# Kernel tuning notes

Hardware: AMD Instinct MI355X
Metric: run time of the kernel (lower is better)

## Reference

```python
import jax, jax.numpy as jnp
import numpy as np

B = 8        # graphs per batch
VG = 20000   # vertices per graph
K = 128      # eigenvectors per graph
D = 128      # channels (C_inout)
V = B * VG


def setup_inputs() -> dict:
    key = jax.random.key(0)
    kx, km, ke, kv, kt = jax.random.split(key, 5)
    x = jax.random.normal(kx, (V, D), dtype=jnp.float32)
    # lumped (diagonal) mass, positive
    mass = jax.random.uniform(km, (V,), dtype=jnp.float32, minval=0.5, maxval=1.5)
    # per-graph nonnegative eigenvalues, sorted within each graph, stacked to (B*K,)
    evals = jnp.sort(jax.random.uniform(ke, (B, K), dtype=jnp.float32) * 10.0, axis=1).reshape(-1)
    # eigenbasis, roughly mass-orthonormal scale
    evecs = jax.random.normal(kv, (V, K), dtype=jnp.float32) / np.sqrt(VG)
    # learned per-channel diffusion times, positive
    diffusion_time = jax.random.uniform(kt, (D,), dtype=jnp.float32, minval=0.01, maxval=0.2)
    batch = jnp.repeat(jnp.arange(B, dtype=jnp.int32), VG)
    return {"x": x, "mass": mass, "evals": evals, "evecs": evecs,
            "diffusion_time": diffusion_time, "batch": batch, "bs": B}


def reference(x, mass, evals, evecs, diffusion_time, batch, bs):
    Vtot, Dc = x.shape
    neig = evals.shape[0] // bs
    vg = Vtot // bs  # equal-sized graphs -> ragged grouped matmul == batched matmul
    t = jnp.maximum(diffusion_time, 1e-8)  # torch clamp(min=1e-8)
    xb = x.reshape(bs, vg, Dc)            # (B, Vg, D)
    eb = evecs.reshape(bs, vg, neig)      # (B, Vg, K)
    mb = mass.reshape(bs, vg)             # (B, Vg) diagonal mass
    # to_basis: basis^T @ (M x) per graph -> (B, K, D)
    x_spec = jnp.einsum('bvk,bvd->bkd', eb * mb[..., None], xb)
    # spectral diffusion coefficients exp(-lambda * t_c): (B, K, D)
    coefs = jnp.exp(-evals.reshape(bs, neig)[..., None] * t[None, None, :])
    # from_basis: evecs @ (coefs * x_spec) per graph -> (B, Vg, D)
    x_diffuse = jnp.einsum('bvk,bkd->bvd', eb, coefs * x_spec)
    return x_diffuse.reshape(Vtot, Dc)
```

## Files before the change

### kernel.cpp

```cpp
#include <hip/hip_runtime.h>

#define BGR 8
#define VG  20000
#define NK  128
#define ND  128

typedef float f32x4 __attribute__((ext_vector_type(4)));
typedef short bf16x8 __attribute__((ext_vector_type(8)));

__device__ __forceinline__ short bf16r(float f) {
    union { float f; unsigned u; } c; c.f = f;
    unsigned r = (c.u + 0x7FFFu + ((c.u >> 16) & 1u)) >> 16;
    return (short)r;
}

#define VC 320
#define S1 40

__global__ __launch_bounds__(256) void k_spec(const float* __restrict__ x,
                                              const float* __restrict__ mass,
                                              const float* __restrict__ evecs,
                                              float* __restrict__ xs) {
    const int g     = blockIdx.y;
    const int chunk = blockIdx.x;
    const int v0    = chunk * VC;
    const int rounds = (VG - v0 < VC ? VG - v0 : VC) >> 5;

    const float* xg = x     + (size_t)g * VG * ND;
    const float* eg = evecs + (size_t)g * VG * NK;
    const float* mg = mass  + (size_t)g * VG;

    __shared__ short At[NK * S1];
    __shared__ short Bt[ND * S1];

    const int tid = threadIdx.x;
    const int l   = tid & 63;
    const int w   = tid >> 6;
    const int lo  = l & 15, hi = l >> 4;
    const int r0  = (w & 1) * 64, c0 = (w >> 1) * 64;

    f32x4 acc[4][4] = {};

    for (int r = 0; r < rounds; ++r) {
        const int vb = v0 + r * 32;
#pragma unroll
        for (int it = 0; it < 8; ++it) {
            const int v = it * 4 + w;
            const float  m  = mg[vb + v];
            const float2 xv = *(const float2*)(xg + (size_t)(vb + v) * ND + 2 * l);
            const float2 ev = *(const float2*)(eg + (size_t)(vb + v) * NK + 2 * l);
            Bt[(2 * l + 0) * S1 + v] = bf16r(xv.x * m);
            Bt[(2 * l + 1) * S1 + v] = bf16r(xv.y * m);
            At[(2 * l + 0) * S1 + v] = bf16r(ev.x);
            At[(2 * l + 1) * S1 + v] = bf16r(ev.y);
        }
        __syncthreads();

        bf16x8 af[4], bfv[4];
#pragma unroll
        for (int i = 0; i < 4; ++i)
            af[i] = *(const bf16x8*)(At + (r0 + 16 * i + lo) * S1 + hi * 8);
#pragma unroll
        for (int j = 0; j < 4; ++j)
            bfv[j] = *(const bf16x8*)(Bt + (c0 + 16 * j + lo) * S1 + hi * 8);
#pragma unroll
        for (int i = 0; i < 4; ++i)
#pragma unroll
            for (int j = 0; j < 4; ++j)
                acc[i][j] = __builtin_amdgcn_mfma_f32_16x16x32_bf16(af[i], bfv[j], acc[i][j], 0, 0, 0);
        __syncthreads();
    }

    float* og = xs + (size_t)g * NK * ND;
#pragma unroll
    for (int i = 0; i < 4; ++i)
#pragma unroll
        for (int j = 0; j < 4; ++j)
#pragma unroll
            for (int t = 0; t < 4; ++t) {
                const int kk = r0 + 16 * i + hi * 4 + t;
                const int dd = c0 + 16 * j + lo;
                atomicAdd(og + kk * ND + dd, acc[i][j][t]);
            }
}

__global__ __launch_bounds__(256) void k_coef(const float* __restrict__ xs,
                                              const float* __restrict__ evals,
                                              const float* __restrict__ dt,
                                              short* __restrict__ Yt) {
    const int gid = blockIdx.x * 256 + threadIdx.x;
    const int g = gid >> 14;
    const int d = (gid >> 7) & 127;
    const int k = gid & 127;
    const float t   = fmaxf(dt[d], 1e-8f);
    const float lam = evals[g * NK + k];
    const float v   = xs[(size_t)g * NK * ND + k * ND + d];
    Yt[gid] = bf16r(__expf(-lam * t) * v);
}

#define S2 128

__global__ __launch_bounds__(256) void k_out(const float* __restrict__ evecs,
                                             const short* __restrict__ Yt,
                                             float* __restrict__ out) {
    const int g     = blockIdx.y;
    const int chunk = blockIdx.x;
    const int v0    = chunk * 128;
    const int rows  = (VG - v0 < 128) ? (VG - v0) : 128;

    const float* eg = evecs + (size_t)g * VG * NK;
    float*       og = out   + (size_t)g * VG * ND;
    const short* yg = Yt    + (size_t)g * ND * NK;

    __shared__ short As[128 * S2];
    __shared__ short Bs[128 * S2];

    const int tid = threadIdx.x;
#pragma unroll
    for (int it = 0; it < 16; ++it) {
        const int id = it * 256 + tid;
        const int v  = id >> 5;
        const int c4 = id & 31;
        const int vc = v < rows ? v : rows - 1;
        const float4 e4 = *(const float4*)(eg + (size_t)(v0 + vc) * NK + 4 * c4);
        short4 p;
        p.x = bf16r(e4.x); p.y = bf16r(e4.y); p.z = bf16r(e4.z); p.w = bf16r(e4.w);
        *(short4*)(As + v * S2 + 4 * c4) = p;
        *(uint2*)(Bs + v * S2 + 4 * c4) = *(const uint2*)(yg + v * NK + 4 * c4);
    }
    __syncthreads();

    const int l  = tid & 63;
    const int w  = tid >> 6;
    const int lo = l & 15, hi = l >> 4;
    const int r0 = (w & 1) * 64, c0 = (w >> 1) * 64;

    f32x4 acc[4][4] = {};
#pragma unroll
    for (int ks = 0; ks < 4; ++ks) {
        const int k0 = ks * 32;
        bf16x8 af[4], bfv[4];
#pragma unroll
        for (int i = 0; i < 4; ++i)
            af[i] = *(const bf16x8*)(As + (r0 + 16 * i + lo) * S2 + k0 + hi * 8);
#pragma unroll
        for (int j = 0; j < 4; ++j)
            bfv[j] = *(const bf16x8*)(Bs + (c0 + 16 * j + lo) * S2 + k0 + hi * 8);
#pragma unroll
        for (int i = 0; i < 4; ++i)
#pragma unroll
            for (int j = 0; j < 4; ++j)
                acc[i][j] = __builtin_amdgcn_mfma_f32_16x16x32_bf16(af[i], bfv[j], acc[i][j], 0, 0, 0);
    }

#pragma unroll
    for (int i = 0; i < 4; ++i)
#pragma unroll
        for (int j = 0; j < 4; ++j)
#pragma unroll
            for (int t = 0; t < 4; ++t) {
                const int vv = r0 + 16 * i + hi * 4 + t;
                if (vv < rows)
                    og[(size_t)(v0 + vv) * ND + c0 + 16 * j + lo] = acc[i][j][t];
            }
}

extern "C" void kernel_launch(void* const* d_in, const int* in_sizes, int n_in,
                              void* d_out, int out_size, void* d_ws, size_t ws_size,
                              hipStream_t stream) {
    const float* x     = (const float*)d_in[0];
    const float* mass  = (const float*)d_in[1];
    const float* evals = (const float*)d_in[2];
    const float* evecs = (const float*)d_in[3];
    const float* dt    = (const float*)d_in[4];
    float* out = (float*)d_out;

    float* xs = (float*)d_ws;
    short* Yt = (short*)((char*)d_ws + (size_t)BGR * NK * ND * 4);

    hipMemsetAsync(d_ws, 0, (size_t)BGR * NK * ND * sizeof(float), stream);

    k_spec<<<dim3((VG + VC - 1) / VC, BGR), 256, 0, stream>>>(x, mass, evecs, xs);
    k_coef<<<(BGR * NK * ND) / 256, 256, 0, stream>>>(xs, evals, dt, Yt);
    k_out<<<dim3((VG + 127) / 128, BGR), 256, 0, stream>>>(evecs, Yt, out);
}
```

Measured before the change: 262.1 us.

## Vectorize spectral staging loads, halve chunk size, read Yt fragments directly from global

In the projection kernel, each thread now loads float4 rows for two adjacent vertices and writes packed bf16 pairs into shared memory, replacing scalar float2 loads and 16-bit stores. The vertex chunk drops from 320 to 160 so twice as many blocks run, at the cost of twice as many atomic flushes of the per-chunk partial results. In the output kernel the Yt operand is no longer staged in shared memory; MFMA fragments are read straight from global/L2, and the evecs tile gets a padded stride to reduce LDS bank conflicts. This removes a shared buffer and a barrier-bound copy but makes each wave issue repeated global reads of the small Yt matrix.

Result: slower. 279.6 us (+6.7%).

```diff
diff --git a/kernel.cpp b/kernel.cpp
--- a/kernel.cpp
+++ b/kernel.cpp
@@ -8,23 +8,23 @@
 typedef float f32x4 __attribute__((ext_vector_type(4)));
 typedef short bf16x8 __attribute__((ext_vector_type(8)));
 
-__device__ __forceinline__ short bf16r(float f) {
+__device__ __forceinline__ unsigned short bf16r(float f) {
     union { float f; unsigned u; } c; c.f = f;
-    unsigned r = (c.u + 0x7FFFu + ((c.u >> 16) & 1u)) >> 16;
-    return (short)r;
+    return (unsigned short)((c.u + 0x7FFFu + ((c.u >> 16) & 1u)) >> 16);
+}
+__device__ __forceinline__ unsigned pack2(float a, float b) {
+    return (unsigned)bf16r(a) | ((unsigned)bf16r(b) << 16);
 }
 
-#define VC 320
+#define VC 160
 #define S1 40
 
 __global__ __launch_bounds__(256) void k_spec(const float* __restrict__ x,
                                               const float* __restrict__ mass,
                                               const float* __restrict__ evecs,
                                               float* __restrict__ xs) {
-    const int g     = blockIdx.y;
-    const int chunk = blockIdx.x;
-    const int v0    = chunk * VC;
-    const int rounds = (VG - v0 < VC ? VG - v0 : VC) >> 5;
+    const int g  = blockIdx.y;
+    const int v0 = blockIdx.x * VC;
 
     const float* xg = x     + (size_t)g * VG * ND;
     const float* eg = evecs + (size_t)g * VG * NK;
@@ -41,18 +41,26 @@
 
     f32x4 acc[4][4] = {};
 
-    for (int r = 0; r < rounds; ++r) {
+#pragma unroll 1
+    for (int r = 0; r < VC / 32; ++r) {
         const int vb = v0 + r * 32;
 #pragma unroll
-        for (int it = 0; it < 8; ++it) {
-            const int v = it * 4 + w;
-            const float  m  = mg[vb + v];
-            const float2 xv = *(const float2*)(xg + (size_t)(vb + v) * ND + 2 * l);
-            const float2 ev = *(const float2*)(eg + (size_t)(vb + v) * NK + 2 * l);
-            Bt[(2 * l + 0) * S1 + v] = bf16r(xv.x * m);
-            Bt[(2 * l + 1) * S1 + v] = bf16r(xv.y * m);
-            At[(2 * l + 0) * S1 + v] = bf16r(ev.x);
-            At[(2 * l + 1) * S1 + v] = bf16r(ev.y);
+        for (int it = 0; it < 2; ++it) {
+            const int id = it * 256 + tid;
+            const int vp = id & 15;
+            const int cq = id >> 4;
+            const int v  = vb + 2 * vp;
+            const float2 mm = *(const float2*)(mg + v);
+            const f32x4 xa = *(const f32x4*)(xg + (size_t)v * ND + 4 * cq);
+            const f32x4 xb = *(const f32x4*)(xg + (size_t)(v + 1) * ND + 4 * cq);
+            const f32x4 ea = *(const f32x4*)(eg + (size_t)v * NK + 4 * cq);
+            const f32x4 eb = *(const f32x4*)(eg + (size_t)(v + 1) * NK + 4 * cq);
+#pragma unroll
+            for (int i = 0; i < 4; ++i) {
+                const int c = 4 * cq + i;
+                *(unsigned*)(Bt + c * S1 + 2 * vp) = pack2(xa[i] * mm.x, xb[i] * mm.y);
+                *(unsigned*)(At + c * S1 + 2 * vp) = pack2(ea[i], eb[i]);
+            }
         }
         __syncthreads();
 
@@ -87,7 +95,7 @@
 __global__ __launch_bounds__(256) void k_coef(const float* __restrict__ xs,
                                               const float* __restrict__ evals,
                                               const float* __restrict__ dt,
-                                              short* __restrict__ Yt) {
+                                              unsigned short* __restrict__ Yt) {
     const int gid = blockIdx.x * 256 + threadIdx.x;
     const int g = gid >> 14;
     const int d = (gid >> 7) & 127;
@@ -98,7 +106,7 @@
     Yt[gid] = bf16r(__expf(-lam * t) * v);
 }
 
-#define S2 128
+#define S2 136
 
 __global__ __launch_bounds__(256) void k_out(const float* __restrict__ evecs,
                                              const short* __restrict__ Yt,
@@ -113,7 +121,6 @@
     const short* yg = Yt    + (size_t)g * ND * NK;
 
     __shared__ short As[128 * S2];
-    __shared__ short Bs[128 * S2];
 
     const int tid = threadIdx.x;
 #pragma unroll
@@ -122,11 +129,11 @@
         const int v  = id >> 5;
         const int c4 = id & 31;
         const int vc = v < rows ? v : rows - 1;
-        const float4 e4 = *(const float4*)(eg + (size_t)(v0 + vc) * NK + 4 * c4);
+        const f32x4 e4 = *(const f32x4*)(eg + (size_t)(v0 + vc) * NK + 4 * c4);
         short4 p;
-        p.x = bf16r(e4.x); p.y = bf16r(e4.y); p.z = bf16r(e4.z); p.w = bf16r(e4.w);
+        p.x = (short)bf16r(e4.x); p.y = (short)bf16r(e4.y);
+        p.z = (short)bf16r(e4.z); p.w = (short)bf16r(e4.w);
         *(short4*)(As + v * S2 + 4 * c4) = p;
-        *(uint2*)(Bs + v * S2 + 4 * c4) = *(const uint2*)(yg + v * NK + 4 * c4);
     }
     __syncthreads();
 
@@ -141,11 +148,11 @@
         const int k0 = ks * 32;
         bf16x8 af[4], bfv[4];
 #pragma unroll
+        for (int j = 0; j < 4; ++j)
+            bfv[j] = *(const bf16x8*)(yg + (size_t)(c0 + 16 * j + lo) * NK + k0 + hi * 8);
+#pragma unroll
         for (int i = 0; i < 4; ++i)
             af[i] = *(const bf16x8*)(As + (r0 + 16 * i + lo) * S2 + k0 + hi * 8);
-#pragma unroll
-        for (int j = 0; j < 4; ++j)
-            bfv[j] = *(const bf16x8*)(Bs + (c0 + 16 * j + lo) * S2 + k0 + hi * 8);
 #pragma unroll
         for (int i = 0; i < 4; ++i)
 #pragma unroll
@@ -175,12 +182,12 @@
     const float* dt    = (const float*)d_in[4];
     float* out = (float*)d_out;
 
-    float* xs = (float*)d_ws;
-    short* Yt = (short*)((char*)d_ws + (size_t)BGR * NK * ND * 4);
+    float*          xs = (float*)d_ws;
+    unsigned short* Yt = (unsigned short*)((char*)d_ws + (size_t)BGR * NK * ND * 4);
 
     hipMemsetAsync(d_ws, 0, (size_t)BGR * NK * ND * sizeof(float), stream);
 
-    k_spec<<<dim3((VG + VC - 1) / VC, BGR), 256, 0, stream>>>(x, mass, evecs, xs);
+    k_spec<<<dim3(VG / VC, BGR), 256, 0, stream>>>(x, mass, evecs, xs);
     k_coef<<<(BGR * NK * ND) / 256, 256, 0, stream>>>(xs, evals, dt, Yt);
-    k_out<<<dim3((VG + 127) / 128, BGR), 256, 0, stream>>>(evecs, Yt, out);
+    k_out<<<dim3((VG + 127) / 128, BGR), 256, 0, stream>>>(evecs, (const short*)Yt, out);
 }
```
